# Kernel optimization log

Measured on AMD Instinct MI355X. Metric: run time of the kernel, lower is better.

## Reference

```python
import jax, jax.numpy as jnp
import numpy as np

R = 131072   # rays
S = 128      # existing samples per ray (existing_bins has S+1 edges)
N_NEW = 64   # new importance samples per ray
HIST_PAD = 1e-5   # NeuSSampler builds PDFSampler(histogram_padding=1e-5)
EPS = 1e-5


def setup_inputs() -> dict:
    key = jax.random.key(0)
    k1, k2, k3, k4 = jax.random.split(key, 4)
    weights = jax.random.uniform(k1, (R, S, 1), dtype=jnp.float32)
    # existing spacing bins must be sorted in [0,1] along the sample axis
    existing_bins = jnp.sort(jax.random.uniform(k2, (R, S + 1), dtype=jnp.float32), axis=-1)
    nears = 0.05 + 0.5 * jax.random.uniform(k3, (R, 1), dtype=jnp.float32)
    fars = nears + 1.0 + 3.0 * jax.random.uniform(k4, (R, 1), dtype=jnp.float32)
    return {"weights": weights, "existing_bins": existing_bins,
            "nears": nears, "fars": fars, "num_samples": N_NEW}


def reference(weights, existing_bins, nears, fars, num_samples):
    # PDFSampler.generate_ray_samples core (eval mode, include_original=False)
    num_bins = num_samples + 1
    w = weights[..., 0] + HIST_PAD                      # [R, S]
    w_sum = jnp.sum(w, axis=-1, keepdims=True)          # [R, 1]
    padding = jax.nn.relu(EPS - w_sum)
    w = w + padding / w.shape[-1]
    w_sum = w_sum + padding
    pdf = w / w_sum                                     # [R, S]
    cdf = jnp.minimum(jnp.ones_like(pdf), jnp.cumsum(pdf, axis=-1))
    cdf = jnp.concatenate([jnp.zeros_like(cdf[..., :1]), cdf], axis=-1)  # [R, S+1]

    # deterministic mid-bin query points (non-stratified branch)
    u = jnp.linspace(0.0, 1.0 - 1.0 / num_bins, num_bins, dtype=cdf.dtype)
    u = u + 1.0 / (2 * num_bins)
    u = jnp.broadcast_to(u, (*cdf.shape[:-1], num_bins))  # [R, num_bins]

    # inverse-CDF: per-ray binary search + gather + linear interp
    inds = jax.vmap(lambda c, q: jnp.searchsorted(c, q, side='right'))(cdf, u)
    last = existing_bins.shape[-1] - 1
    below = jnp.clip(inds - 1, 0, last)
    above = jnp.clip(inds, 0, last)
    cdf_g0 = jnp.take_along_axis(cdf, below, axis=-1)
    bins_g0 = jnp.take_along_axis(existing_bins, below, axis=-1)
    cdf_g1 = jnp.take_along_axis(cdf, above, axis=-1)
    bins_g1 = jnp.take_along_axis(existing_bins, above, axis=-1)
    t = jnp.clip(jnp.nan_to_num((u - cdf_g0) / (cdf_g1 - cdf_g0), nan=0.0,
                                posinf=0.0, neginf=0.0), 0.0, 1.0)
    bins = bins_g0 + t * (bins_g1 - bins_g0)            # [R, num_bins]
    bins = jax.lax.stop_gradient(bins)                  # torch: bins.detach()

    # spacing_to_euclidean_fn for UniformSampler: x*s_far + (1-x)*s_near
    euclidean_bins = bins * fars + (1.0 - bins) * nears  # [R, num_bins]
    return euclidean_bins
```

## Files before the change

kernel.cpp:

```cpp
#include <hip/hip_runtime.h>


#define DPP_FADD(x, ctrl, rmask)                                             \
    ((x) + __int_as_float(__builtin_amdgcn_update_dpp(                       \
               0, __float_as_int(x), (ctrl), (rmask), 0xf, true)))

__global__ __launch_bounds__(256) void neus_sampler_kernel(
    const float* __restrict__ weights,
    const float* __restrict__ bins_g,
    const float* __restrict__ nears,
    const float* __restrict__ fars,
    float* __restrict__ out,
    int R)
{
    constexpr int S  = 128;
    constexpr int NB = 65;
    constexpr float HPAD = 1e-5f;

    const int lane = threadIdx.x & 63;
    const int ray  = blockIdx.x * 4 + (threadIdx.x >> 6);
    if (ray >= R) return;
    const int uray = __builtin_amdgcn_readfirstlane(ray);

    const float2 wpair =
        reinterpret_cast<const float2*>(weights + (size_t)uray * S)[lane];
    const float* brow = bins_g + (size_t)uray * (S + 1);
    const float2 bpair = reinterpret_cast<const float2*>(brow)[lane];
    const float b_last = brow[S];

    const float w1 = wpair.y + HPAD;
    float ps = (wpair.x + HPAD) + w1;

    ps = DPP_FADD(ps, 0x111, 0xf);
    ps = DPP_FADD(ps, 0x112, 0xf);
    ps = DPP_FADD(ps, 0x114, 0xf);
    ps = DPP_FADD(ps, 0x118, 0xf);
    ps = DPP_FADD(ps, 0x142, 0xa);
    ps = DPP_FADD(ps, 0x143, 0xc);

    const float total =
        __int_as_float(__builtin_amdgcn_readlane(__float_as_int(ps), 63));
    const float padding = fmaxf(1e-5f - total, 0.0f);
    const float padc    = padding * (1.0f / S);
    const float inv     = __builtin_amdgcn_rcpf(total + padding);

    const float c_hi  = fminf(1.0f, fmaf((float)(2 * lane + 2), padc, ps) * inv);
    const float c_mid = fminf(1.0f, fmaf((float)(2 * lane + 1), padc, ps - w1) * inv);
    float c_lo = __shfl_up(c_hi, 1, 64);
    if (lane == 0) c_lo = 0.0f;
    float b2 = __shfl_down(bpair.x, 1, 64);
    if (lane == 63) b2 = b_last;

    const float nearv = nears[uray];
    const float farv  = fars[uray];
    const float fmn   = farv - nearv;
    float* orow = out + (size_t)uray * NB;

    auto jf = [](float c) -> int {
        int j = (int)ceilf(fmaf(65.0f, c, -0.5f));
        return j < 0 ? 0 : (j > NB ? NB : j);
    };

    const int j0 = jf(c_lo);
    const int j2 = (lane == 63) ? NB : jf(c_hi);
    int j1 = jf(c_mid);
    j1 = j1 < j0 ? j0 : (j1 > j2 ? j2 : j1);

    if (j1 > j0) {
        const float r  = __builtin_amdgcn_rcpf(c_mid - c_lo);
        const float dt = r * (1.0f / 65.0f);
        const float bd = bpair.y - bpair.x;
        float u = (float)(2 * j0 + 1) * (1.0f / 130.0f);
        float t = (u - c_lo) * r;
        for (int j = j0; j < j1; ++j) {
            const float tc = fminf(fmaxf(t, 0.0f), 1.0f);
            orow[j] = fmaf(fmaf(tc, bd, bpair.x), fmn, nearv);
            t += dt;
        }
    }
    if (j2 > j1) {
        const float r  = __builtin_amdgcn_rcpf(c_hi - c_mid);
        const float dt = r * (1.0f / 65.0f);
        const float bd = b2 - bpair.y;
        float u = (float)(2 * j1 + 1) * (1.0f / 130.0f);
        float t = (u - c_mid) * r;
        for (int j = j1; j < j2; ++j) {
            const float tc = fminf(fmaxf(t, 0.0f), 1.0f);
            orow[j] = fmaf(fmaf(tc, bd, bpair.y), fmn, nearv);
            t += dt;
        }
    }
}

extern "C" void kernel_launch(void* const* d_in, const int* in_sizes, int n_in,
                              void* d_out, int out_size, void* d_ws, size_t ws_size,
                              hipStream_t stream) {
    const float* weights = (const float*)d_in[0];
    const float* ebins   = (const float*)d_in[1];
    const float* nears   = (const float*)d_in[2];
    const float* fars    = (const float*)d_in[3];
    float* out = (float*)d_out;
    const int R = in_sizes[0] / 128;
    const int blocks = (R + 3) / 4;
    hipLaunchKernelGGL(neus_sampler_kernel, dim3(blocks), dim3(256), 0, stream,
                       weights, ebins, nears, fars, out, R);
}
```

Baseline: 163.2 us.

## Process two rays per wavefront with four CDF segments per lane

Each 64-lane wavefront now handles two rays, 32 lanes per ray. Each lane loads four weights as a float4 plus four bin edges, computes a local prefix, and runs a 32-lane DPP scan in place of the full 64-lane scan. Each lane then writes samples for up to four CDF segments, and the grid is halved to match. The aim is fewer wavefronts and less per-ray scan and launch overhead, in exchange for more divergent serial segment loops per lane and bin loads that are no longer vector-aligned (the row stride is 129 floats).

```diff
diff --git a/kernel.cpp b/kernel.cpp
--- a/kernel.cpp
+++ b/kernel.cpp
@@ -14,82 +14,96 @@
     int R)
 {
     constexpr int S  = 128;
+    constexpr int SE = 129;
     constexpr int NB = 65;
     constexpr float HPAD = 1e-5f;
 
     const int lane = threadIdx.x & 63;
-    const int ray  = blockIdx.x * 4 + (threadIdx.x >> 6);
-    if (ray >= R) return;
-    const int uray = __builtin_amdgcn_readfirstlane(ray);
+    const int m    = lane & 31;
+    const int wb   = blockIdx.x * 4 + (threadIdx.x >> 6);
+    const int rayA = wb * 2;
+    if (rayA >= R) return;
+    const int ray  = rayA + (lane >> 5);
+    const bool ok  = ray < R;
+    const int cray = ok ? ray : rayA;
 
-    const float2 wpair =
-        reinterpret_cast<const float2*>(weights + (size_t)uray * S)[lane];
-    const float* brow = bins_g + (size_t)uray * (S + 1);
-    const float2 bpair = reinterpret_cast<const float2*>(brow)[lane];
+    const float4 wq =
+        reinterpret_cast<const float4*>(weights + (size_t)cray * S)[m];
+    const float* brow = bins_g + (size_t)cray * SE;
+    const float bx = brow[4 * m];
+    const float by = brow[4 * m + 1];
+    const float bz = brow[4 * m + 2];
+    const float bw = brow[4 * m + 3];
     const float b_last = brow[S];
+    const float nearv = nears[cray];
+    const float farv  = fars[cray];
 
-    const float w1 = wpair.y + HPAD;
-    float ps = (wpair.x + HPAD) + w1;
+    const float w0 = wq.x + HPAD, w1 = wq.y + HPAD;
+    const float w2 = wq.z + HPAD, w3 = wq.w + HPAD;
+    const float p1 = w0, p2 = w0 + w1, p3 = p2 + w2, p4 = p3 + w3;
 
-    ps = DPP_FADD(ps, 0x111, 0xf);
-    ps = DPP_FADD(ps, 0x112, 0xf);
-    ps = DPP_FADD(ps, 0x114, 0xf);
-    ps = DPP_FADD(ps, 0x118, 0xf);
-    ps = DPP_FADD(ps, 0x142, 0xa);
-    ps = DPP_FADD(ps, 0x143, 0xc);
+    float sc = p4;
+    sc = DPP_FADD(sc, 0x111, 0xf);
+    sc = DPP_FADD(sc, 0x112, 0xf);
+    sc = DPP_FADD(sc, 0x114, 0xf);
+    sc = DPP_FADD(sc, 0x118, 0xf);
+    sc = DPP_FADD(sc, 0x142, 0xa);
 
-    const float total =
-        __int_as_float(__builtin_amdgcn_readlane(__float_as_int(ps), 63));
+    const float tA =
+        __int_as_float(__builtin_amdgcn_readlane(__float_as_int(sc), 31));
+    const float tB =
+        __int_as_float(__builtin_amdgcn_readlane(__float_as_int(sc), 63));
+    const float total   = (lane < 32) ? tA : tB;
     const float padding = fmaxf(1e-5f - total, 0.0f);
     const float padc    = padding * (1.0f / S);
     const float inv     = __builtin_amdgcn_rcpf(total + padding);
+    const float excl    = sc - p4;
 
-    const float c_hi  = fminf(1.0f, fmaf((float)(2 * lane + 2), padc, ps) * inv);
-    const float c_mid = fminf(1.0f, fmaf((float)(2 * lane + 1), padc, ps - w1) * inv);
-    float c_lo = __shfl_up(c_hi, 1, 64);
-    if (lane == 0) c_lo = 0.0f;
-    float b2 = __shfl_down(bpair.x, 1, 64);
-    if (lane == 63) b2 = b_last;
+    const float mb = (float)(4 * m);
+    const float e1 = fminf(1.0f, fmaf(mb + 1.0f, padc, excl + p1) * inv);
+    const float e2 = fminf(1.0f, fmaf(mb + 2.0f, padc, excl + p2) * inv);
+    const float e3 = fminf(1.0f, fmaf(mb + 3.0f, padc, excl + p3) * inv);
+    const float e4 = fminf(1.0f, fmaf(mb + 4.0f, padc, excl + p4) * inv);
 
-    const float nearv = nears[uray];
-    const float farv  = fars[uray];
-    const float fmn   = farv - nearv;
-    float* orow = out + (size_t)uray * NB;
+    float e0 = __shfl_up(e4, 1, 64);
+    if (m == 0) e0 = 0.0f;
+    float b4 = __shfl_down(bx, 1, 64);
+    if (m == 31) b4 = b_last;
 
     auto jf = [](float c) -> int {
         int j = (int)ceilf(fmaf(65.0f, c, -0.5f));
         return j < 0 ? 0 : (j > NB ? NB : j);
     };
 
-    const int j0 = jf(c_lo);
-    const int j2 = (lane == 63) ? NB : jf(c_hi);
-    int j1 = jf(c_mid);
-    j1 = j1 < j0 ? j0 : (j1 > j2 ? j2 : j1);
+    int j0 = jf(e0);
+    int j4 = (m == 31) ? NB : jf(e4);
+    if (!ok) { j0 = 0; j4 = 0; }
+    j4 = j4 < j0 ? j0 : j4;
+    int j1 = jf(e1); j1 = j1 < j0 ? j0 : (j1 > j4 ? j4 : j1);
+    int j2 = jf(e2); j2 = j2 < j1 ? j1 : (j2 > j4 ? j4 : j2);
+    int j3 = jf(e3); j3 = j3 < j2 ? j2 : (j3 > j4 ? j4 : j3);
 
-    if (j1 > j0) {
-        const float r  = __builtin_amdgcn_rcpf(c_mid - c_lo);
-        const float dt = r * (1.0f / 65.0f);
-        const float bd = bpair.y - bpair.x;
-        float u = (float)(2 * j0 + 1) * (1.0f / 130.0f);
-        float t = (u - c_lo) * r;
-        for (int j = j0; j < j1; ++j) {
-            const float tc = fminf(fmaxf(t, 0.0f), 1.0f);
-            orow[j] = fmaf(fmaf(tc, bd, bpair.x), fmn, nearv);
-            t += dt;
+    const float fmn = farv - nearv;
+    float* orow = out + (size_t)cray * NB;
+
+    auto seg = [&](float clo, float chi, float b0, float b1, int js, int je) {
+        if (je > js) {
+            const float r  = __builtin_amdgcn_rcpf(chi - clo);
+            const float dt = r * (1.0f / 65.0f);
+            const float bd = b1 - b0;
+            float t = (fmaf((float)(2 * js + 1), (1.0f / 130.0f), -clo)) * r;
+            for (int j = js; j < je; ++j) {
+                const float tc = fminf(fmaxf(t, 0.0f), 1.0f);
+                orow[j] = fmaf(fmaf(tc, bd, b0), fmn, nearv);
+                t += dt;
+            }
         }
-    }
-    if (j2 > j1) {
-        const float r  = __builtin_amdgcn_rcpf(c_hi - c_mid);
-        const float dt = r * (1.0f / 65.0f);
-        const float bd = b2 - bpair.y;
-        float u = (float)(2 * j1 + 1) * (1.0f / 130.0f);
-        float t = (u - c_mid) * r;
-        for (int j = j1; j < j2; ++j) {
-            const float tc = fminf(fmaxf(t, 0.0f), 1.0f);
-            orow[j] = fmaf(fmaf(tc, bd, bpair.y), fmn, nearv);
-            t += dt;
-        }
-    }
+    };
+
+    seg(e0, e1, bx, by, j0, j1);
+    seg(e1, e2, by, bz, j1, j2);
+    seg(e2, e3, bz, bw, j2, j3);
+    seg(e3, e4, bw, b4, j3, j4);
 }
 
 extern "C" void kernel_launch(void* const* d_in, const int* in_sizes, int n_in,
@@ -101,7 +115,7 @@
     const float* fars    = (const float*)d_in[3];
     float* out = (float*)d_out;
     const int R = in_sizes[0] / 128;
-    const int blocks = (R + 3) / 4;
+    const int blocks = (R + 7) / 8;
     hipLaunchKernelGGL(neus_sampler_kernel, dim3(blocks), dim3(256), 0, stream,
                        weights, ebins, nears, fars, out, R);
 }
```

After: 164.2 us. Within noise of the previous version (+0.6%).

## Process four rays per wave with LDS segment map for coalesced output writes

Applied to the files above, without the earlier changes.

Each wave now handles four rays, issuing all their global loads up front to increase memory-level parallelism. The per-lane variable-length scatter loops are replaced by an LDS cdf/bin staging step: an atomicMax segment map plus a DPP prefix-max tells each output lane its bracketing CDF index, so every lane writes exactly one output element contiguously. This removes divergent strided stores but adds LDS traffic, atomics and wave barriers, and it reduces the grid size by a factor of four.

```diff
diff --git a/kernel.cpp b/kernel.cpp
--- a/kernel.cpp
+++ b/kernel.cpp
@@ -5,7 +5,19 @@
     ((x) + __int_as_float(__builtin_amdgcn_update_dpp(                       \
                0, __float_as_int(x), (ctrl), (rmask), 0xf, true)))
 
-__global__ __launch_bounds__(256) void neus_sampler_kernel(
+#define DPP_IMAX(x, ctrl, rmask)                                             \
+    do {                                                                     \
+        int _y = __builtin_amdgcn_update_dpp(0, (x), (ctrl), (rmask), 0xf,   \
+                                             true);                          \
+        (x) = (x) > _y ? (x) : _y;                                           \
+    } while (0)
+
+__device__ __forceinline__ void lds_fence() {
+    __builtin_amdgcn_s_waitcnt(0xC07F);
+    __builtin_amdgcn_wave_barrier();
+}
+
+__global__ __launch_bounds__(256, 8) void neus_sampler_kernel(
     const float* __restrict__ weights,
     const float* __restrict__ bins_g,
     const float* __restrict__ nears,
@@ -14,80 +26,113 @@
     int R)
 {
     constexpr int S  = 128;
+    constexpr int SE = 129;
     constexpr int NB = 65;
+    constexpr int NR = 4;
     constexpr float HPAD = 1e-5f;
 
+    __shared__ float s_cdf[4][2][132];
+    __shared__ float s_bin[4][2][132];
+    __shared__ int   s_seg[4][2][68];
+
     const int lane = threadIdx.x & 63;
-    const int ray  = blockIdx.x * 4 + (threadIdx.x >> 6);
-    if (ray >= R) return;
-    const int uray = __builtin_amdgcn_readfirstlane(ray);
+    const int wv   = threadIdx.x >> 6;
+    const int uw   = __builtin_amdgcn_readfirstlane(blockIdx.x * 4 + wv);
+    const int base = uw * NR;
+    if (base >= R) return;
 
-    const float2 wpair =
-        reinterpret_cast<const float2*>(weights + (size_t)uray * S)[lane];
-    const float* brow = bins_g + (size_t)uray * (S + 1);
-    const float2 bpair = reinterpret_cast<const float2*>(brow)[lane];
-    const float b_last = brow[S];
-
-    const float w1 = wpair.y + HPAD;
-    float ps = (wpair.x + HPAD) + w1;
-
-    ps = DPP_FADD(ps, 0x111, 0xf);
-    ps = DPP_FADD(ps, 0x112, 0xf);
-    ps = DPP_FADD(ps, 0x114, 0xf);
-    ps = DPP_FADD(ps, 0x118, 0xf);
-    ps = DPP_FADD(ps, 0x142, 0xa);
-    ps = DPP_FADD(ps, 0x143, 0xc);
-
-    const float total =
-        __int_as_float(__builtin_amdgcn_readlane(__float_as_int(ps), 63));
-    const float padding = fmaxf(1e-5f - total, 0.0f);
-    const float padc    = padding * (1.0f / S);
-    const float inv     = __builtin_amdgcn_rcpf(total + padding);
-
-    const float c_hi  = fminf(1.0f, fmaf((float)(2 * lane + 2), padc, ps) * inv);
-    const float c_mid = fminf(1.0f, fmaf((float)(2 * lane + 1), padc, ps - w1) * inv);
-    float c_lo = __shfl_up(c_hi, 1, 64);
-    if (lane == 0) c_lo = 0.0f;
-    float b2 = __shfl_down(bpair.x, 1, 64);
-    if (lane == 63) b2 = b_last;
-
-    const float nearv = nears[uray];
-    const float farv  = fars[uray];
-    const float fmn   = farv - nearv;
-    float* orow = out + (size_t)uray * NB;
+    float2 W[NR], B[NR];
+    float  BL[NR], NE[NR], FA[NR];
+    #pragma unroll
+    for (int i = 0; i < NR; ++i) {
+        int r = base + i; r = r < R ? r : R - 1;
+        W[i] = reinterpret_cast<const float2*>(weights + (size_t)r * S)[lane];
+        const float* brow = bins_g + (size_t)r * SE;
+        B[i]  = reinterpret_cast<const float2*>(brow)[lane];
+        BL[i] = brow[S];
+        NE[i] = nears[r];
+        FA[i] = fars[r];
+    }
 
     auto jf = [](float c) -> int {
         int j = (int)ceilf(fmaf(65.0f, c, -0.5f));
         return j < 0 ? 0 : (j > NB ? NB : j);
     };
 
-    const int j0 = jf(c_lo);
-    const int j2 = (lane == 63) ? NB : jf(c_hi);
-    int j1 = jf(c_mid);
-    j1 = j1 < j0 ? j0 : (j1 > j2 ? j2 : j1);
+    #pragma unroll
+    for (int i = 0; i < NR; ++i) {
+        const int ray = base + i;
+        const bool ok = ray < R;
+        float* cdfb = s_cdf[wv][i & 1];
+        float* binb = s_bin[wv][i & 1];
+        int*   segb = s_seg[wv][i & 1];
 
-    if (j1 > j0) {
-        const float r  = __builtin_amdgcn_rcpf(c_mid - c_lo);
-        const float dt = r * (1.0f / 65.0f);
-        const float bd = bpair.y - bpair.x;
-        float u = (float)(2 * j0 + 1) * (1.0f / 130.0f);
-        float t = (u - c_lo) * r;
-        for (int j = j0; j < j1; ++j) {
-            const float tc = fminf(fmaxf(t, 0.0f), 1.0f);
-            orow[j] = fmaf(fmaf(tc, bd, bpair.x), fmn, nearv);
-            t += dt;
-        }
-    }
-    if (j2 > j1) {
-        const float r  = __builtin_amdgcn_rcpf(c_hi - c_mid);
-        const float dt = r * (1.0f / 65.0f);
-        const float bd = b2 - bpair.y;
-        float u = (float)(2 * j1 + 1) * (1.0f / 130.0f);
-        float t = (u - c_mid) * r;
-        for (int j = j1; j < j2; ++j) {
-            const float tc = fminf(fmaxf(t, 0.0f), 1.0f);
-            orow[j] = fmaf(fmaf(tc, bd, bpair.y), fmn, nearv);
-            t += dt;
+        segb[lane] = 0;
+        if (lane == 0) segb[64] = 0;
+
+        const float w1 = W[i].y + HPAD;
+        float ps = (W[i].x + HPAD) + w1;
+        ps = DPP_FADD(ps, 0x111, 0xf);
+        ps = DPP_FADD(ps, 0x112, 0xf);
+        ps = DPP_FADD(ps, 0x114, 0xf);
+        ps = DPP_FADD(ps, 0x118, 0xf);
+        ps = DPP_FADD(ps, 0x142, 0xa);
+        ps = DPP_FADD(ps, 0x143, 0xc);
+
+        const float total = __int_as_float(
+            __builtin_amdgcn_readlane(__float_as_int(ps), 63));
+        const float padding = fmaxf(1e-5f - total, 0.0f);
+        const float padc    = padding * (1.0f / S);
+        const float inv     = __builtin_amdgcn_rcpf(total + padding);
+
+        const float c_hi  = fminf(1.0f, fmaf((float)(2*lane+2), padc, ps) * inv);
+        const float c_mid = fminf(1.0f, fmaf((float)(2*lane+1), padc, ps - w1) * inv);
+        float b2 = __shfl_down(B[i].x, 1, 64);
+        if (lane == 63) b2 = BL[i];
+
+        cdfb[2*lane+1] = c_mid;
+        cdfb[2*lane+2] = c_hi;
+        binb[2*lane+1] = B[i].y;
+        binb[2*lane+2] = b2;
+        if (lane == 0) { cdfb[0] = 0.0f; binb[0] = B[i].x; }
+
+        __builtin_amdgcn_wave_barrier();
+
+        const int jm = jf(c_mid);
+        const int jh = jf(c_hi);
+        if (jm < NB) atomicMax(&segb[jm], 2*lane+1);
+        if (jh < NB) atomicMax(&segb[jh], 2*lane+2);
+
+        lds_fence();
+
+        int k = segb[lane];
+        DPP_IMAX(k, 0x111, 0xf);
+        DPP_IMAX(k, 0x112, 0xf);
+        DPP_IMAX(k, 0x114, 0xf);
+        DPP_IMAX(k, 0x118, 0xf);
+        DPP_IMAX(k, 0x142, 0xa);
+        DPP_IMAX(k, 0x143, 0xc);
+        const int k63 = __builtin_amdgcn_readlane(k, 63);
+        const int s64 = segb[64];
+        const int k64 = k63 > s64 ? k63 : s64;
+
+        const float fmn = FA[i] - NE[i];
+        auto interp = [&](int kk, float u) -> float {
+            const int kb = (kk + 1 > S) ? S : kk + 1;
+            const float c0 = cdfb[kk], c1 = cdfb[kb];
+            const float b0 = binb[kk], b1 = binb[kb];
+            float t = (u - c0) * __builtin_amdgcn_rcpf(c1 - c0);
+            t = fminf(fmaxf(t, 0.0f), 1.0f);
+            return fmaf(fmaf(t, b1 - b0, b0), fmn, NE[i]);
+        };
+
+        const float res = interp(k,   (float)(2*lane+1) * (1.0f / 130.0f));
+        const float r64 = interp(k64, 129.0f * (1.0f / 130.0f));
+
+        if (ok) {
+            float* orow = out + (size_t)ray * NB;
+            orow[lane] = res;
+            if (lane == 0) orow[NB - 1] = r64;
         }
     }
 }
@@ -101,7 +146,8 @@
     const float* fars    = (const float*)d_in[3];
     float* out = (float*)d_out;
     const int R = in_sizes[0] / 128;
-    const int blocks = (R + 3) / 4;
+    const int rays_per_block = 4 * 4;
+    const int blocks = (R + rays_per_block - 1) / rays_per_block;
     hipLaunchKernelGGL(neus_sampler_kernel, dim3(blocks), dim3(256), 0, stream,
                        weights, ebins, nears, fars, out, R);
 }
```

Result: slower. 167.0 us (+2.3%).

## Use persistent grid-stride waves with register prefetch of next ray

Applied to the files above, without the earlier changes.

Replaces the one-ray-per-wave launch with a fixed grid of 2048 blocks where each wave loops over rays in grid-stride order. Each iteration loads the next ray's weights, bins, near and far into registers before processing the current ray, so memory latency can overlap compute and stores. This reduces launch and wave-setup overhead but lowers the number of waves in flight and adds register pressure.

```diff
diff --git a/kernel.cpp b/kernel.cpp
--- a/kernel.cpp
+++ b/kernel.cpp
@@ -14,81 +14,98 @@
     int R)
 {
     constexpr int S  = 128;
+    constexpr int SE = 129;
     constexpr int NB = 65;
     constexpr float HPAD = 1e-5f;
 
     const int lane = threadIdx.x & 63;
-    const int ray  = blockIdx.x * 4 + (threadIdx.x >> 6);
-    if (ray >= R) return;
-    const int uray = __builtin_amdgcn_readfirstlane(ray);
-
-    const float2 wpair =
-        reinterpret_cast<const float2*>(weights + (size_t)uray * S)[lane];
-    const float* brow = bins_g + (size_t)uray * (S + 1);
-    const float2 bpair = reinterpret_cast<const float2*>(brow)[lane];
-    const float b_last = brow[S];
-
-    const float w1 = wpair.y + HPAD;
-    float ps = (wpair.x + HPAD) + w1;
-
-    ps = DPP_FADD(ps, 0x111, 0xf);
-    ps = DPP_FADD(ps, 0x112, 0xf);
-    ps = DPP_FADD(ps, 0x114, 0xf);
-    ps = DPP_FADD(ps, 0x118, 0xf);
-    ps = DPP_FADD(ps, 0x142, 0xa);
-    ps = DPP_FADD(ps, 0x143, 0xc);
-
-    const float total =
-        __int_as_float(__builtin_amdgcn_readlane(__float_as_int(ps), 63));
-    const float padding = fmaxf(1e-5f - total, 0.0f);
-    const float padc    = padding * (1.0f / S);
-    const float inv     = __builtin_amdgcn_rcpf(total + padding);
-
-    const float c_hi  = fminf(1.0f, fmaf((float)(2 * lane + 2), padc, ps) * inv);
-    const float c_mid = fminf(1.0f, fmaf((float)(2 * lane + 1), padc, ps - w1) * inv);
-    float c_lo = __shfl_up(c_hi, 1, 64);
-    if (lane == 0) c_lo = 0.0f;
-    float b2 = __shfl_down(bpair.x, 1, 64);
-    if (lane == 63) b2 = b_last;
-
-    const float nearv = nears[uray];
-    const float farv  = fars[uray];
-    const float fmn   = farv - nearv;
-    float* orow = out + (size_t)uray * NB;
+    const int gw   = blockIdx.x * 4 + (threadIdx.x >> 6);
+    const int nw   = gridDim.x * 4;
 
     auto jf = [](float c) -> int {
         int j = (int)ceilf(fmaf(65.0f, c, -0.5f));
         return j < 0 ? 0 : (j > NB ? NB : j);
     };
 
-    const int j0 = jf(c_lo);
-    const int j2 = (lane == 63) ? NB : jf(c_hi);
-    int j1 = jf(c_mid);
-    j1 = j1 < j0 ? j0 : (j1 > j2 ? j2 : j1);
+    float2 W, Bp;
+    float  BL, NE, FA;
 
-    if (j1 > j0) {
-        const float r  = __builtin_amdgcn_rcpf(c_mid - c_lo);
-        const float dt = r * (1.0f / 65.0f);
-        const float bd = bpair.y - bpair.x;
-        float u = (float)(2 * j0 + 1) * (1.0f / 130.0f);
-        float t = (u - c_lo) * r;
-        for (int j = j0; j < j1; ++j) {
-            const float tc = fminf(fmaxf(t, 0.0f), 1.0f);
-            orow[j] = fmaf(fmaf(tc, bd, bpair.x), fmn, nearv);
-            t += dt;
+    int ray = gw;
+    if (ray < R) {
+        const int ur = __builtin_amdgcn_readfirstlane(ray);
+        W = reinterpret_cast<const float2*>(weights + (size_t)ur * S)[lane];
+        const float* brow = bins_g + (size_t)ur * SE;
+        Bp = reinterpret_cast<const float2*>(brow)[lane];
+        BL = brow[S]; NE = nears[ur]; FA = fars[ur];
+    }
+
+    while (ray < R) {
+        const int nray = ray + nw;
+        float2 W2, B2; float BL2, NE2, FA2;
+        if (nray < R) {
+            const int ur2 = __builtin_amdgcn_readfirstlane(nray);
+            W2 = reinterpret_cast<const float2*>(weights + (size_t)ur2 * S)[lane];
+            const float* brow2 = bins_g + (size_t)ur2 * SE;
+            B2 = reinterpret_cast<const float2*>(brow2)[lane];
+            BL2 = brow2[S]; NE2 = nears[ur2]; FA2 = fars[ur2];
         }
-    }
-    if (j2 > j1) {
-        const float r  = __builtin_amdgcn_rcpf(c_hi - c_mid);
-        const float dt = r * (1.0f / 65.0f);
-        const float bd = b2 - bpair.y;
-        float u = (float)(2 * j1 + 1) * (1.0f / 130.0f);
-        float t = (u - c_mid) * r;
-        for (int j = j1; j < j2; ++j) {
-            const float tc = fminf(fmaxf(t, 0.0f), 1.0f);
-            orow[j] = fmaf(fmaf(tc, bd, bpair.y), fmn, nearv);
-            t += dt;
+
+        const int ur = __builtin_amdgcn_readfirstlane(ray);
+        const float w1 = W.y + HPAD;
+        float ps = (W.x + HPAD) + w1;
+        ps = DPP_FADD(ps, 0x111, 0xf);
+        ps = DPP_FADD(ps, 0x112, 0xf);
+        ps = DPP_FADD(ps, 0x114, 0xf);
+        ps = DPP_FADD(ps, 0x118, 0xf);
+        ps = DPP_FADD(ps, 0x142, 0xa);
+        ps = DPP_FADD(ps, 0x143, 0xc);
+
+        const float total = __int_as_float(
+            __builtin_amdgcn_readlane(__float_as_int(ps), 63));
+        const float padding = fmaxf(1e-5f - total, 0.0f);
+        const float padc    = padding * (1.0f / S);
+        const float inv     = __builtin_amdgcn_rcpf(total + padding);
+
+        const float c_hi  = fminf(1.0f, fmaf((float)(2*lane+2), padc, ps) * inv);
+        const float c_mid = fminf(1.0f, fmaf((float)(2*lane+1), padc, ps - w1) * inv);
+        float c_lo = __shfl_up(c_hi, 1, 64);
+        if (lane == 0) c_lo = 0.0f;
+        float b2 = __shfl_down(Bp.x, 1, 64);
+        if (lane == 63) b2 = BL;
+
+        const int j0 = jf(c_lo);
+        const int j2 = (lane == 63) ? NB : jf(c_hi);
+        int j1 = jf(c_mid);
+        j1 = j1 < j0 ? j0 : (j1 > j2 ? j2 : j1);
+
+        const float fmn = FA - NE;
+        float* orow = out + (size_t)ur * NB;
+
+        if (j1 > j0) {
+            const float r  = __builtin_amdgcn_rcpf(c_mid - c_lo);
+            const float dt = r * (1.0f / 65.0f);
+            const float bd = Bp.y - Bp.x;
+            float t = fmaf((float)(2*j0+1), (1.0f/130.0f), -c_lo) * r;
+            for (int j = j0; j < j1; ++j) {
+                const float tc = fminf(fmaxf(t, 0.0f), 1.0f);
+                orow[j] = fmaf(fmaf(tc, bd, Bp.x), fmn, NE);
+                t += dt;
+            }
         }
+        if (j2 > j1) {
+            const float r  = __builtin_amdgcn_rcpf(c_hi - c_mid);
+            const float dt = r * (1.0f / 65.0f);
+            const float bd = b2 - Bp.y;
+            float t = fmaf((float)(2*j1+1), (1.0f/130.0f), -c_mid) * r;
+            for (int j = j1; j < j2; ++j) {
+                const float tc = fminf(fmaxf(t, 0.0f), 1.0f);
+                orow[j] = fmaf(fmaf(tc, bd, Bp.y), fmn, NE);
+                t += dt;
+            }
+        }
+
+        ray = nray;
+        W = W2; Bp = B2; BL = BL2; NE = NE2; FA = FA2;
     }
 }
 
@@ -101,7 +118,7 @@
     const float* fars    = (const float*)d_in[3];
     float* out = (float*)d_out;
     const int R = in_sizes[0] / 128;
-    const int blocks = (R + 3) / 4;
+    const int blocks = 2048;
     hipLaunchKernelGGL(neus_sampler_kernel, dim3(blocks), dim3(256), 0, stream,
                        weights, ebins, nears, fars, out, R);
 }
```

Result: slower. 171.4 us (+5.0%).
